# Performance work log

Hardware: AMD Instinct MI355X
Metric: run time of the kernel (lower is better)

The kernel has to match this reference:

```python
import jax, jax.numpy as jnp
import numpy as np
from jax import lax

N = 512  # neurons (== input features in this base class)

@jax.custom_vjp
def spike_fn(x):
    # Heaviside spike with fast-sigmoid surrogate gradient (standard for LIF SNNs)
    return (x > 0.0).astype(x.dtype)

def _spike_fwd(x):
    return spike_fn(x), x

def _spike_bwd(x, g):
    sg = 1.0 / (1.0 + 10.0 * jnp.abs(x)) ** 2
    return (g * sg,)

spike_fn.defvjp(_spike_fwd, _spike_bwd)

def setup_inputs() -> dict:
    key = jax.random.key(0)
    k1, k2, k3, k4, k5, k6 = jax.random.split(key, 6)
    B, T = 64, 1000
    scale = 1.0 / np.sqrt(N)
    return {
        "input_batch": jax.random.normal(k1, (B, T, N), dtype=jnp.float32),
        "state_snn": jnp.zeros((2, B, N), dtype=jnp.float32),  # [v; s]
        "state_LI": jnp.zeros((B, N), dtype=jnp.float32),
        "W1": jax.random.normal(k2, (N, N), dtype=jnp.float32) * scale,
        "W2": jax.random.normal(k3, (N, N), dtype=jnp.float32) * scale,
        "leak_v": jax.random.uniform(k4, (N,), dtype=jnp.float32, minval=0.8, maxval=0.99),
        "leak_i": jax.random.uniform(k5, (N,), dtype=jnp.float32, minval=0.8, maxval=0.99),
        "thresh": jax.random.uniform(k6, (N,), dtype=jnp.float32, minval=0.5, maxval=1.5),
    }

def reference(input_batch, state_snn, state_LI, W1, W2, leak_v, leak_i, thresh):
    # input_batch: [B, T, N]; time loop expressed as lax.scan over T
    v0, s0 = state_snn[0], state_snn[1]
    xs = jnp.swapaxes(input_batch, 0, 1)  # [T, B, N]

    def step(carry, x_t):
        v, s, u = carry
        ff = x_t @ W1.T                        # LIF feed-forward current
        v = leak_v * v * (1.0 - s) + ff        # leak + reset-to-zero on spike
        s = spike_fn(v - thresh)               # spike generation
        u = leak_i * u + s @ W2.T              # leaky-integrator readout
        return (v, s, u), (s, jnp.stack([v, s]), u)

    _, (spikes, states_snn, decoded) = lax.scan(step, (v0, s0, state_LI), xs)
    # spikes: [T,B,N], states_snn: [T,2,B,N], decoded: [T,B,N]
    return spikes, states_snn, decoded
```

## Files before the change

kernel.cpp:

```cpp
#include <hip/hip_runtime.h>

#define T_STEPS 1000
#define B_SZ 64
#define N_SZ 512
#define BN_TOT (B_SZ * N_SZ)
#define TBN   ((size_t)T_STEPS * BN_TOT)

typedef __attribute__((ext_vector_type(4))) float f32x4;
typedef __attribute__((ext_vector_type(8))) short bf16x8;
typedef unsigned short ushort_t;

__global__ __launch_bounds__(256, 4)
void sgemm_abt(const float* __restrict__ A, const float* __restrict__ W,
               float* __restrict__ C)
{
    constexpr int K = 512;
    constexpr int BK = 16;
    constexpr int LDT = 128 + 4;
    __shared__ float As[BK][LDT];
    __shared__ float Bs[BK][LDT];

    const int tid = threadIdx.x;
    const int tx = tid & 15;
    const int ty = tid >> 4;
    const size_t m0 = (size_t)blockIdx.y * 128;
    const int n0 = blockIdx.x * 128;

    float acc[8][8];
#pragma unroll
    for (int i = 0; i < 8; ++i)
#pragma unroll
        for (int j = 0; j < 8; ++j) acc[i][j] = 0.0f;

    for (int k0 = 0; k0 < K; k0 += BK) {
#pragma unroll
        for (int p = 0; p < 2; ++p) {
            int i = tid + p * 256;
            int r = i >> 2;
            int q = i & 3;
            float4 va = *(const float4*)(A + (m0 + r) * K + k0 + q * 4);
            As[q * 4 + 0][r] = va.x; As[q * 4 + 1][r] = va.y;
            As[q * 4 + 2][r] = va.z; As[q * 4 + 3][r] = va.w;
            float4 vb = *(const float4*)(W + (size_t)(n0 + r) * K + k0 + q * 4);
            Bs[q * 4 + 0][r] = vb.x; Bs[q * 4 + 1][r] = vb.y;
            Bs[q * 4 + 2][r] = vb.z; Bs[q * 4 + 3][r] = vb.w;
        }
        __syncthreads();
#pragma unroll
        for (int k = 0; k < BK; ++k) {
            float a[8], b[8];
            *(float4*)&a[0] = *(const float4*)&As[k][ty * 8];
            *(float4*)&a[4] = *(const float4*)&As[k][ty * 8 + 4];
            *(float4*)&b[0] = *(const float4*)&Bs[k][tx * 4];
            *(float4*)&b[4] = *(const float4*)&Bs[k][tx * 4 + 64];
#pragma unroll
            for (int i = 0; i < 8; ++i)
#pragma unroll
                for (int j = 0; j < 8; ++j)
                    acc[i][j] = fmaf(a[i], b[j], acc[i][j]);
        }
        __syncthreads();
    }

#pragma unroll
    for (int i = 0; i < 8; ++i) {
        float* cp = C + (m0 + ty * 8 + i) * 512 + n0 + tx * 4;
        *(float4*)cp        = make_float4(acc[i][0], acc[i][1], acc[i][2], acc[i][3]);
        *(float4*)(cp + 64) = make_float4(acc[i][4], acc[i][5], acc[i][6], acc[i][7]);
    }
}

__global__ __launch_bounds__(256)
void w2_split(const float* __restrict__ W2, ushort_t* __restrict__ Wc)
{
    int i = blockIdx.x * 256 + threadIdx.x;
    unsigned wb = __float_as_uint(W2[i]);
    unsigned rne = wb + 0x7FFFu + ((wb >> 16) & 1u);
    Wc[i] = (ushort_t)(rne >> 16);
}

__device__ __forceinline__ uint4 mexp8(unsigned bb)
{
    uint4 r;
    r.x = ((bb) & 1u) * 0x3F80u        | (((bb) >> 1) & 1u) * 0x3F800000u;
    r.y = (((bb) >> 2) & 1u) * 0x3F80u | (((bb) >> 3) & 1u) * 0x3F800000u;
    r.z = (((bb) >> 4) & 1u) * 0x3F80u | (((bb) >> 5) & 1u) * 0x3F800000u;
    r.w = (((bb) >> 6) & 1u) * 0x3F80u | (((bb) >> 7) & 1u) * 0x3F800000u;
    return r;
}

__global__ __launch_bounds__(256, 2)
void gemm2_mfma(const unsigned* __restrict__ Msk, const ushort_t* __restrict__ Wc,
                float* __restrict__ C)
{
    constexpr int NT = 512 / 32;
    __shared__ ushort_t As[2][128 * 32];
    __shared__ ushort_t Bs[2][128 * 32];

    const int tid = threadIdx.x;
    const int m0 = blockIdx.y * 128;
    const int n0 = blockIdx.x * 128;
    const int wid = tid >> 6;
    const int lane = tid & 63;
    const int wm = (wid >> 1) * 64;
    const int wn = (wid & 1) * 64;
    const int fr = lane & 15;
    const int fq = lane >> 4;

    f32x4 acc[4][4] = {};

    const int rA = tid >> 2;
    const int cA = (tid & 3) * 8;
    const size_t mrow0 = (size_t)(m0 + (tid >> 2)) * 16;
    const size_t mrow1 = (size_t)(m0 + 64 + (tid >> 2)) * 16;
    const int qsh = (tid & 3) * 8;

    unsigned mw0, mw1;

#define STAGE_B(buf, t)                                                      \
    {                                                                        \
        const int k0_ = (t) * 32;                                            \
        _Pragma("unroll")                                                    \
        for (int i = 0; i < 2; ++i) {                                        \
            __builtin_amdgcn_global_load_lds(                                \
                (const __attribute__((address_space(1))) unsigned int*)      \
                    (Wc + (size_t)(n0 + i * 64 + rA) * 512 + k0_ + cA),      \
                (__attribute__((address_space(3))) unsigned int*)            \
                    (Bs[buf] + i * 2048 + tid * 8),                          \
                16, 0, 0);                                                   \
        }                                                                    \
    }
#define MLOAD(t)                                                             \
    {                                                                        \
        const int mword = (t);             \
        mw0 = Msk[mrow0 + mword];                                            \
        mw1 = Msk[mrow1 + mword];                                            \
    }
#define MSTORE(buf)                                                          \
    {                                                                        \
        *(uint4*)(As[buf] + tid * 8)        = mexp8((mw0 >> qsh) & 0xFFu);   \
        *(uint4*)(As[buf] + 2048 + tid * 8) = mexp8((mw1 >> qsh) & 0xFFu);   \
    }

    MLOAD(0);
    STAGE_B(0, 0);
    MSTORE(0);
    asm volatile("s_waitcnt vmcnt(0)" ::: "memory");
    __syncthreads();

    int cur = 0;
    for (int t = 0; t < NT; ++t) {
        if (t + 1 < NT) {
            MLOAD(t + 1);
            STAGE_B(cur ^ 1, t + 1);
        }

        bf16x8 a[4], b[4];
#pragma unroll
        for (int m = 0; m < 4; ++m)
            a[m] = *(const bf16x8*)(As[cur] + (wm + m * 16 + fr) * 32 + fq * 8);
#pragma unroll
        for (int n = 0; n < 4; ++n)
            b[n] = *(const bf16x8*)(Bs[cur] + (wn + n * 16 + fr) * 32 + fq * 8);
#pragma unroll
        for (int m = 0; m < 4; ++m)
#pragma unroll
            for (int n = 0; n < 4; ++n)
                acc[m][n] = __builtin_amdgcn_mfma_f32_16x16x32_bf16(
                    a[m], b[n], acc[m][n], 0, 0, 0);

        if (t + 1 < NT)
            MSTORE(cur ^ 1);

        asm volatile("s_waitcnt vmcnt(0)" ::: "memory");
        __syncthreads();
        cur ^= 1;
    }
#undef STAGE_B
#undef MLOAD
#undef MSTORE

#pragma unroll
    for (int m = 0; m < 4; ++m) {
        const int row = m0 + wm + m * 16 + fq * 4;
#pragma unroll
        for (int n = 0; n < 4; ++n) {
            const int col = n0 + wn + n * 16 + fr;
#pragma unroll
            for (int j = 0; j < 4; ++j)
                C[(size_t)(row + j) * 512 + col] = acc[m][n][j];
        }
    }
}

__global__ __launch_bounds__(128)
void lif_scan(const float* __restrict__ ff, const float* __restrict__ st0,
              const float* __restrict__ leak_v, const float* __restrict__ thresh,
              float* __restrict__ spikes, float* __restrict__ states,
              unsigned long long* __restrict__ Msk)
{
    const int idx = blockIdx.x * 128 + threadIdx.x;
    const int n = idx & (N_SZ - 1);
    const int b = idx >> 9;

    float v = st0[idx];
    float s = st0[BN_TOT + idx];
    const float lv = leak_v[n];
    const float th = thresh[n];

    const float* fp = ff + (size_t)b * T_STEPS * N_SZ + n;
    float* sp  = spikes + idx;
    float* stp = states + idx;
    const int wslot = idx >> 6;
    const bool wlead = ((threadIdx.x & 63) == 0);

    float f[8];
#pragma unroll
    for (int j = 0; j < 8; ++j) f[j] = fp[(size_t)j * N_SZ];

    for (int t = 0; t < T_STEPS; t += 8) {
        float g[8];
#pragma unroll
        for (int j = 0; j < 8; ++j) g[j] = 0.f;
        if (t + 8 < T_STEPS) {
            const float* q = fp + (size_t)(t + 8) * N_SZ;
#pragma unroll
            for (int j = 0; j < 8; ++j) g[j] = q[(size_t)j * N_SZ];
        }
#pragma unroll
        for (int j = 0; j < 8; ++j) {
            v = lv * v * (1.0f - s) + f[j];
            s = (v > th) ? 1.0f : 0.0f;
            size_t o  = (size_t)(t + j) * BN_TOT;
            size_t o2 = (size_t)(t + j) * (2 * BN_TOT);
            sp[o] = s;
            stp[o2] = v;
            stp[o2 + BN_TOT] = s;
            unsigned long long bm = __ballot(s != 0.0f);
            if (Msk && wlead)
                Msk[(size_t)(t + j) * 512 + wslot] = bm;
        }
#pragma unroll
        for (int j = 0; j < 8; ++j) f[j] = g[j];
    }
}

__global__ __launch_bounds__(128)
void li_scan(float* __restrict__ dec, const float* __restrict__ u0,
             const float* __restrict__ leak_i)
{
    const int idx = blockIdx.x * 128 + threadIdx.x;
    const int n = idx & (N_SZ - 1);

    float u = u0[idx];
    const float li = leak_i[n];
    float* p = dec + idx;

    float y[8];
#pragma unroll
    for (int j = 0; j < 8; ++j) y[j] = p[(size_t)j * BN_TOT];

    for (int t = 0; t < T_STEPS; t += 8) {
        float g[8];
#pragma unroll
        for (int j = 0; j < 8; ++j) g[j] = 0.f;
        if (t + 8 < T_STEPS) {
            float* q = p + (size_t)(t + 8) * BN_TOT;
#pragma unroll
            for (int j = 0; j < 8; ++j) g[j] = q[(size_t)j * BN_TOT];
        }
#pragma unroll
        for (int j = 0; j < 8; ++j) {
            u = fmaf(li, u, y[j]);
            p[(size_t)(t + j) * BN_TOT] = u;
        }
#pragma unroll
        for (int j = 0; j < 8; ++j) y[j] = g[j];
    }
}

extern "C" void kernel_launch(void* const* d_in, const int* in_sizes, int n_in,
                              void* d_out, int out_size, void* d_ws, size_t ws_size,
                              hipStream_t stream)
{
    (void)in_sizes; (void)n_in; (void)out_size;

    const float* X     = (const float*)d_in[0];
    const float* st_sn = (const float*)d_in[1];
    const float* st_li = (const float*)d_in[2];
    const float* W1    = (const float*)d_in[3];
    const float* W2    = (const float*)d_in[4];
    const float* lv    = (const float*)d_in[5];
    const float* li    = (const float*)d_in[6];
    const float* th    = (const float*)d_in[7];

    float* spikes = (float*)d_out;
    float* states = spikes + TBN;
    float* dec    = states + 2 * TBN;

    const size_t WS_NEED = (size_t)512 * 512 * 2 + (size_t)1000 * 512 * 8;
    const bool use_mfma = (ws_size >= WS_NEED);
    ushort_t* Wc = (ushort_t*)d_ws;
    unsigned long long* Msk = (unsigned long long*)(Wc + (size_t)512 * 512);

    const dim3 gemm_grid(4, 500), gemm_block(256);
    const dim3 scan_grid(BN_TOT / 128), scan_block(128);

    if (use_mfma)
        w2_split<<<dim3(1024), dim3(256), 0, stream>>>(W2, Wc);

    sgemm_abt<<<gemm_grid, gemm_block, 0, stream>>>(X, W1, dec);

    lif_scan<<<scan_grid, scan_block, 0, stream>>>(dec, st_sn, lv, th,
                                                   spikes, states,
                                                   use_mfma ? Msk
                                                            : (unsigned long long*)0);

    if (use_mfma)
        gemm2_mfma<<<gemm_grid, gemm_block, 0, stream>>>((const unsigned*)Msk,
                                                         Wc, dec);
    else
        sgemm_abt<<<gemm_grid, gemm_block, 0, stream>>>(spikes, W2, dec);

    li_scan<<<scan_grid, scan_block, 0, stream>>>(dec, st_li, li);
}
```

Before: 691.1 us.

## Fuse spike-weight MFMA GEMM with leaky-integrator scan per batch column tile

Replaces the separate bf16 MFMA GEMM and the li_scan kernel with one kernel. Each block owns one batch element and a 128-column slice, and walks time in 128-step chunks. After each chunk it runs the leaky-integrator recurrence in registers, passing the carry across lanes with shuffles, and writes only the final decoded output. This removes the full write and re-read of the intermediate GEMM result. In exchange the grid shrinks from 2000 blocks to 256 and adds a serial per-chunk scan, so parallelism and latency hiding drop. The mask workspace is padded to 1024 timesteps.

New measurement: 724.1 us. +4.8%, slower.

```diff
diff --git a/kernel.cpp b/kernel.cpp
--- a/kernel.cpp
+++ b/kernel.cpp
@@ -90,56 +90,62 @@
 }
 
 __global__ __launch_bounds__(256, 2)
-void gemm2_mfma(const unsigned* __restrict__ Msk, const ushort_t* __restrict__ Wc,
-                float* __restrict__ C)
-{
-    constexpr int NT = 512 / 32;
+void gemm2_li_fused(const unsigned* __restrict__ Msk,
+                    const ushort_t* __restrict__ Wc,
+                    const float* __restrict__ u0v,
+                    const float* __restrict__ leak_i,
+                    float* __restrict__ dec)
+{
     __shared__ ushort_t As[2][128 * 32];
     __shared__ ushort_t Bs[2][128 * 32];
 
     const int tid = threadIdx.x;
-    const int m0 = blockIdx.y * 128;
     const int n0 = blockIdx.x * 128;
+    const int b  = blockIdx.y;
     const int wid = tid >> 6;
     const int lane = tid & 63;
-    const int wm = (wid >> 1) * 64;
-    const int wn = (wid & 1) * 64;
     const int fr = lane & 15;
     const int fq = lane >> 4;
-
-    f32x4 acc[4][4] = {};
-
-    const int rA = tid >> 2;
-    const int cA = (tid & 3) * 8;
-    const size_t mrow0 = (size_t)(m0 + (tid >> 2)) * 16;
-    const size_t mrow1 = (size_t)(m0 + 64 + (tid >> 2)) * 16;
-    const int qsh = (tid & 3) * 8;
-
-    unsigned mw0, mw1;
-
-#define STAGE_B(buf, t)                                                      \
+    const int wn = wid * 32;
+
+    const int rB = tid >> 2;
+    const int cB = (tid & 3) * 8;
+    const int arow = tid >> 1;
+    const int ahalf = tid & 1;
+
+    const int col0 = n0 + wn + fr;
+    const int col1 = col0 + 16;
+    const float li0 = leak_i[col0];
+    const float li1 = leak_i[col1];
+    float u0 = u0v[b * 512 + col0];
+    float u1 = u0v[b * 512 + col1];
+
+    f32x4 acc[8][2] = {};
+    unsigned mword;
+
+#define MLOAD(it)                                                            \
     {                                                                        \
-        const int k0_ = (t) * 32;                                            \
+        const int tt_ = ((it) >> 4) * 128 + arow;                            \
+        mword = Msk[(size_t)tt_ * 1024 + b * 16 + ((it) & 15)];              \
+    }
+#define STAGE_B(buf, it)                                                     \
+    {                                                                        \
+        const int k0_ = ((it) & 15) * 32;                                    \
         _Pragma("unroll")                                                    \
         for (int i = 0; i < 2; ++i) {                                        \
             __builtin_amdgcn_global_load_lds(                                \
                 (const __attribute__((address_space(1))) unsigned int*)      \
-                    (Wc + (size_t)(n0 + i * 64 + rA) * 512 + k0_ + cA),      \
+                    (Wc + (size_t)(n0 + i * 64 + rB) * 512 + k0_ + cB),      \
                 (__attribute__((address_space(3))) unsigned int*)            \
                     (Bs[buf] + i * 2048 + tid * 8),                          \
                 16, 0, 0);                                                   \
         }                                                                    \
     }
-#define MLOAD(t)                                                             \
-    {                                                                        \
-        const int mword = (t);             \
-        mw0 = Msk[mrow0 + mword];                                            \
-        mw1 = Msk[mrow1 + mword];                                            \
-    }
 #define MSTORE(buf)                                                          \
     {                                                                        \
-        *(uint4*)(As[buf] + tid * 8)        = mexp8((mw0 >> qsh) & 0xFFu);   \
-        *(uint4*)(As[buf] + 2048 + tid * 8) = mexp8((mw1 >> qsh) & 0xFFu);   \
+        unsigned h_ = (mword >> (ahalf * 16)) & 0xFFFFu;                     \
+        *(uint4*)(As[buf] + arow * 32 + ahalf * 16)     = mexp8(h_ & 0xFFu); \
+        *(uint4*)(As[buf] + arow * 32 + ahalf * 16 + 8) = mexp8(h_ >> 8);    \
     }
 
     MLOAD(0);
@@ -149,48 +155,66 @@
     __syncthreads();
 
     int cur = 0;
-    for (int t = 0; t < NT; ++t) {
-        if (t + 1 < NT) {
-            MLOAD(t + 1);
-            STAGE_B(cur ^ 1, t + 1);
-        }
-
-        bf16x8 a[4], b[4];
-#pragma unroll
-        for (int m = 0; m < 4; ++m)
-            a[m] = *(const bf16x8*)(As[cur] + (wm + m * 16 + fr) * 32 + fq * 8);
-#pragma unroll
-        for (int n = 0; n < 4; ++n)
-            b[n] = *(const bf16x8*)(Bs[cur] + (wn + n * 16 + fr) * 32 + fq * 8);
-#pragma unroll
-        for (int m = 0; m < 4; ++m)
-#pragma unroll
-            for (int n = 0; n < 4; ++n)
+    for (int it = 0; it < 128; ++it) {
+        if (it + 1 < 128) {
+            MLOAD(it + 1);
+            STAGE_B(cur ^ 1, it + 1);
+        }
+
+        bf16x8 a[8], bb[2];
+#pragma unroll
+        for (int m = 0; m < 8; ++m)
+            a[m] = *(const bf16x8*)(As[cur] + (m * 16 + fr) * 32 + fq * 8);
+#pragma unroll
+        for (int n = 0; n < 2; ++n)
+            bb[n] = *(const bf16x8*)(Bs[cur] + (wn + n * 16 + fr) * 32 + fq * 8);
+#pragma unroll
+        for (int m = 0; m < 8; ++m)
+#pragma unroll
+            for (int n = 0; n < 2; ++n)
                 acc[m][n] = __builtin_amdgcn_mfma_f32_16x16x32_bf16(
-                    a[m], b[n], acc[m][n], 0, 0, 0);
-
-        if (t + 1 < NT)
+                    a[m], bb[n], acc[m][n], 0, 0, 0);
+
+        if (it + 1 < 128)
             MSTORE(cur ^ 1);
+
+        if ((it & 15) == 15) {
+            const int cb = (it >> 4) * 128;
+#pragma unroll
+            for (int m = 0; m < 8; ++m) {
+#pragma unroll
+                for (int q = 0; q < 4; ++q) {
+                    const int tb = cb + m * 16 + q * 4;
+                    if (fq == q) {
+#pragma unroll
+                        for (int j = 0; j < 4; ++j) {
+                            if (tb + j < T_STEPS) {
+                                u0 = fmaf(li0, u0, acc[m][0][j]);
+                                u1 = fmaf(li1, u1, acc[m][1][j]);
+                                size_t o = (size_t)(tb + j) * BN_TOT + b * 512;
+                                dec[o + col0] = u0;
+                                dec[o + col1] = u1;
+                            }
+                        }
+                    }
+                    u0 = __shfl(u0, q * 16 + fr);
+                    u1 = __shfl(u1, q * 16 + fr);
+                }
+            }
+#pragma unroll
+            for (int m = 0; m < 8; ++m) {
+                acc[m][0] = (f32x4){0.f, 0.f, 0.f, 0.f};
+                acc[m][1] = (f32x4){0.f, 0.f, 0.f, 0.f};
+            }
+        }
 
         asm volatile("s_waitcnt vmcnt(0)" ::: "memory");
         __syncthreads();
         cur ^= 1;
     }
+#undef MLOAD
 #undef STAGE_B
-#undef MLOAD
 #undef MSTORE
-
-#pragma unroll
-    for (int m = 0; m < 4; ++m) {
-        const int row = m0 + wm + m * 16 + fq * 4;
-#pragma unroll
-        for (int n = 0; n < 4; ++n) {
-            const int col = n0 + wn + n * 16 + fr;
-#pragma unroll
-            for (int j = 0; j < 4; ++j)
-                C[(size_t)(row + j) * 512 + col] = acc[m][n][j];
-        }
-    }
 }
 
 __global__ __launch_bounds__(128)
@@ -298,7 +322,7 @@
     float* states = spikes + TBN;
     float* dec    = states + 2 * TBN;
 
-    const size_t WS_NEED = (size_t)512 * 512 * 2 + (size_t)1000 * 512 * 8;
+    const size_t WS_NEED = (size_t)512 * 512 * 2 + (size_t)1024 * 512 * 8;
     const bool use_mfma = (ws_size >= WS_NEED);
     ushort_t* Wc = (ushort_t*)d_ws;
     unsigned long long* Msk = (unsigned long long*)(Wc + (size_t)512 * 512);
@@ -316,11 +340,11 @@
                                                    use_mfma ? Msk
                                                             : (unsigned long long*)0);
 
-    if (use_mfma)
-        gemm2_mfma<<<gemm_grid, gemm_block, 0, stream>>>((const unsigned*)Msk,
-                                                         Wc, dec);
-    else
+    if (use_mfma) {
+        gemm2_li_fused<<<dim3(4, 64), dim3(256), 0, stream>>>(
+            (const unsigned*)Msk, Wc, st_li, li, dec);
+    } else {
         sgemm_abt<<<gemm_grid, gemm_block, 0, stream>>>(spikes, W2, dec);
-
-    li_scan<<<scan_grid, scan_block, 0, stream>>>(dec, st_li, li);
-}
+        li_scan<<<scan_grid, scan_block, 0, stream>>>(dec, st_li, li);
+    }
+}
```
